# Kernel tuning notes

Measured on AMD Instinct MI355X. Metric: run time of the kernel, lower is better.

The kernel has to match this reference:

```python
import jax, jax.numpy as jnp
import numpy as np

CLASSES = 128
M_IN = 64
N_OUT = 32
N_SAMPLES = 65536


def setup_inputs() -> dict:
    key = jax.random.key(0)
    k1, k2, k3, k4 = jax.random.split(key, 4)
    x = jax.random.normal(k1, (N_SAMPLES, M_IN), dtype=jnp.float32)
    inds = jax.random.randint(k2, (N_SAMPLES,), 0, CLASSES, dtype=jnp.int64)
    # Conv2d(in=M_IN, out=CLASSES*N_OUT, kernel=1) -> weight (CLASSES*N_OUT, M_IN), bias (CLASSES*N_OUT,)
    bound = 1.0 / np.sqrt(M_IN)
    W = jax.random.uniform(k3, (CLASSES * N_OUT, M_IN), minval=-bound, maxval=bound, dtype=jnp.float32)
    b = jax.random.uniform(k4, (CLASSES * N_OUT,), minval=-bound, maxval=bound, dtype=jnp.float32)
    return {"x": x, "inds": inds, "W": W, "b": b}


def reference(x, inds, W, b):
    # 1x1 conv == GEMM: (N, m) @ (m, classes*n) + bias -> (N, classes*n)
    y = jnp.einsum("nm,cm->nc", x, W) + b  # (N, classes*n_out)
    y = y.reshape(-1, CLASSES, N_OUT)       # (N, classes, n_out)
    # gather the selected class slice per sample
    idx = inds.astype(jnp.int32)[:, None, None]  # (N, 1, 1)
    out = jnp.take_along_axis(y, jnp.broadcast_to(idx, (y.shape[0], 1, N_OUT)), axis=1)
    return out.reshape(-1, N_OUT)
```

## Files before the change

kernel.cpp:

```cpp
#include <hip/hip_runtime.h>

#define CLASSES    128
#define M_IN       64
#define N_OUT      32
#define N_SAMPLES  65536
#define BUCKET_CAP N_SAMPLES

typedef __attribute__((ext_vector_type(8))) short bf16x8;
typedef __attribute__((ext_vector_type(4))) float f32x4;

__device__ inline short f2bf(float f) {
    unsigned u = __builtin_bit_cast(unsigned, f);
    u += 0x7fffu + ((u >> 16) & 1u);
    return (short)(u >> 16);
}

__device__ inline bf16x8 cvt8(const float4 a, const float4 b) {
    bf16x8 r;
    r[0] = f2bf(a.x); r[1] = f2bf(a.y); r[2] = f2bf(a.z); r[3] = f2bf(a.w);
    r[4] = f2bf(b.x); r[5] = f2bf(b.y); r[6] = f2bf(b.z); r[7] = f2bf(b.w);
    return r;
}

__global__ __launch_bounds__(128) void zero_cnt_kernel(int* __restrict__ cnt) {
    cnt[threadIdx.x] = 0;
}

__global__ __launch_bounds__(256) void scatter_kernel(
    const int* __restrict__ inds,
    int*       __restrict__ cnt,
    int*       __restrict__ bucket)
{
    __shared__ int lcnt[CLASSES];
    __shared__ int lbase[CLASSES];
    const int tid = threadIdx.x;
    if (tid < CLASSES) lcnt[tid] = 0;
    __syncthreads();

    const int i    = blockIdx.x * 256 + tid;
    const int c    = inds[i];
    const int lpos = atomicAdd(&lcnt[c], 1);
    __syncthreads();

    if (tid < CLASSES) lbase[tid] = atomicAdd(&cnt[tid], lcnt[tid]);
    __syncthreads();

    bucket[c * BUCKET_CAP + lbase[c] + lpos] = i;
}

__global__ __launch_bounds__(256) void compute_kernel(
    const float* __restrict__ x,
    const float* __restrict__ W,
    const float* __restrict__ b,
    const int*   __restrict__ cnt,
    const int*   __restrict__ bucket,
    float*       __restrict__ out)
{
    const int c    = blockIdx.x >> 3;
    const int j8   = blockIdx.x & 7;
    const int wv   = threadIdx.x >> 6;
    const int lane = threadIdx.x & 63;
    const int m16  = lane & 15;
    const int quad = lane >> 4;

    bf16x8 Bf[2][2];
#pragma unroll
    for (int nh = 0; nh < 2; ++nh)
#pragma unroll
        for (int kh = 0; kh < 2; ++kh) {
            const float* p = W + (size_t)(c * N_OUT + nh * 16 + m16) * M_IN
                               + kh * 32 + quad * 8;
            Bf[nh][kh] = cvt8(*(const float4*)p, *(const float4*)(p + 4));
        }

    const float b0 = b[c * N_OUT + m16];
    const float b1 = b[c * N_OUT + 16 + m16];

    const int cn = cnt[c];
    if (cn == 0) return;
    const int T = (cn + 15) >> 4;
    const int* bk = bucket + c * BUCKET_CAP;

    for (int t = j8 * 4 + wv; t < T; t += 32) {
        const int base = t << 4;

        const int pa = base + m16;
        const int na = bk[(pa < cn) ? pa : (cn - 1)];
        const float* xr = x + (size_t)na * M_IN + quad * 8;
        const bf16x8 A0 = cvt8(*(const float4*)xr,        *(const float4*)(xr + 4));
        const bf16x8 A1 = cvt8(*(const float4*)(xr + 32), *(const float4*)(xr + 36));

        f32x4 acc0 = {0.f, 0.f, 0.f, 0.f};
        f32x4 acc1 = {0.f, 0.f, 0.f, 0.f};
        acc0 = __builtin_amdgcn_mfma_f32_16x16x32_bf16(A0, Bf[0][0], acc0, 0, 0, 0);
        acc0 = __builtin_amdgcn_mfma_f32_16x16x32_bf16(A1, Bf[0][1], acc0, 0, 0, 0);
        acc1 = __builtin_amdgcn_mfma_f32_16x16x32_bf16(A0, Bf[1][0], acc1, 0, 0, 0);
        acc1 = __builtin_amdgcn_mfma_f32_16x16x32_bf16(A1, Bf[1][1], acc1, 0, 0, 0);

#pragma unroll
        for (int r = 0; r < 4; ++r) {
            const int p = base + quad * 4 + r;
            if (p < cn) {
                const int n = bk[p];
                out[(size_t)n * N_OUT + m16]      = acc0[r] + b0;
                out[(size_t)n * N_OUT + 16 + m16] = acc1[r] + b1;
            }
        }
    }
}

extern "C" void kernel_launch(void* const* d_in, const int* in_sizes, int n_in,
                              void* d_out, int out_size, void* d_ws, size_t ws_size,
                              hipStream_t stream) {
    const float* x    = (const float*)d_in[0];
    const int*   inds = (const int*)  d_in[1];
    const float* W    = (const float*)d_in[2];
    const float* b    = (const float*)d_in[3];
    float*       out  = (float*)d_out;

    int* cnt    = (int*)d_ws;
    int* bucket = (int*)d_ws + 1024;

    zero_cnt_kernel<<<1, 128, 0, stream>>>(cnt);
    scatter_kernel<<<N_SAMPLES / 256, 256, 0, stream>>>(inds, cnt, bucket);
    compute_kernel<<<CLASSES * 8, 256, 0, stream>>>(x, W, b, cnt, bucket, out);
}
```

Baseline: 83.97 us.

## Prefetch next tile in compute loop, halve grids, vectorize scatter, memset counters

The compute kernel now loads the next tile's gathered x rows before it runs the MFMAs and stores for the current tile, a software-pipelining step meant to hide gather latency. The compute grid drops to 4 blocks per class, so each wave handles more tiles. The scatter kernel reads two indices per thread as an int2, and the zero-counter kernel becomes hipMemsetAsync. The int2 read treats the int64 index buffer as pairs of int32, which only works if the indices really arrive as int32. Fewer blocks may also reduce latency hiding.

```diff
diff --git a/kernel.cpp b/kernel.cpp
--- a/kernel.cpp
+++ b/kernel.cpp
@@ -22,10 +22,6 @@
     return r;
 }
 
-__global__ __launch_bounds__(128) void zero_cnt_kernel(int* __restrict__ cnt) {
-    cnt[threadIdx.x] = 0;
-}
-
 __global__ __launch_bounds__(256) void scatter_kernel(
     const int* __restrict__ inds,
     int*       __restrict__ cnt,
@@ -37,15 +33,18 @@
     if (tid < CLASSES) lcnt[tid] = 0;
     __syncthreads();
 
-    const int i    = blockIdx.x * 256 + tid;
-    const int c    = inds[i];
-    const int lpos = atomicAdd(&lcnt[c], 1);
+    const int  vi = blockIdx.x * 256 + tid;
+    const int2 cc = reinterpret_cast<const int2*>(inds)[vi];
+    const int  i0 = vi * 2, i1 = i0 + 1;
+    const int  p0 = atomicAdd(&lcnt[cc.x], 1);
+    const int  p1 = atomicAdd(&lcnt[cc.y], 1);
     __syncthreads();
 
     if (tid < CLASSES) lbase[tid] = atomicAdd(&cnt[tid], lcnt[tid]);
     __syncthreads();
 
-    bucket[c * BUCKET_CAP + lbase[c] + lpos] = i;
+    bucket[cc.x * BUCKET_CAP + lbase[cc.x] + p0] = i0;
+    bucket[cc.y * BUCKET_CAP + lbase[cc.y] + p1] = i1;
 }
 
 __global__ __launch_bounds__(256) void compute_kernel(
@@ -56,12 +55,15 @@
     const int*   __restrict__ bucket,
     float*       __restrict__ out)
 {
-    const int c    = blockIdx.x >> 3;
-    const int j8   = blockIdx.x & 7;
+    const int c    = blockIdx.x >> 2;
+    const int j4   = blockIdx.x & 3;
     const int wv   = threadIdx.x >> 6;
     const int lane = threadIdx.x & 63;
     const int m16  = lane & 15;
     const int quad = lane >> 4;
+
+    const int  cn = cnt[c];
+    const int* bk = bucket + c * BUCKET_CAP;
 
     bf16x8 Bf[2][2];
 #pragma unroll
@@ -72,24 +74,40 @@
                                + kh * 32 + quad * 8;
             Bf[nh][kh] = cvt8(*(const float4*)p, *(const float4*)(p + 4));
         }
-
     const float b0 = b[c * N_OUT + m16];
     const float b1 = b[c * N_OUT + 16 + m16];
 
-    const int cn = cnt[c];
     if (cn == 0) return;
     const int T = (cn + 15) >> 4;
-    const int* bk = bucket + c * BUCKET_CAP;
+    int t = j4 * 4 + wv;
+    if (t >= T) return;
 
-    for (int t = j8 * 4 + wv; t < T; t += 32) {
-        const int base = t << 4;
+    int base = t << 4;
+    {
+    }
+    int pa = base + m16;
+    int na = bk[(pa < cn) ? pa : (cn - 1)];
+    const float* xr = x + (size_t)na * M_IN + quad * 8;
+    float4 xa0 = *(const float4*)xr,        xa1 = *(const float4*)(xr + 4);
+    float4 xa2 = *(const float4*)(xr + 32), xa3 = *(const float4*)(xr + 36);
 
-        const int pa = base + m16;
-        const int na = bk[(pa < cn) ? pa : (cn - 1)];
-        const float* xr = x + (size_t)na * M_IN + quad * 8;
-        const bf16x8 A0 = cvt8(*(const float4*)xr,        *(const float4*)(xr + 4));
-        const bf16x8 A1 = cvt8(*(const float4*)(xr + 32), *(const float4*)(xr + 36));
+    while (true) {
+        const int  tn   = t + 16;
+        const bool more = tn < T;
 
+        int base_n = base, na_n = na;
+        float4 xb0 = xa0, xb1 = xa1, xb2 = xa2, xb3 = xa3;
+        if (more) {
+            base_n = tn << 4;
+            const int pan = base_n + m16;
+            na_n = bk[(pan < cn) ? pan : (cn - 1)];
+            const float* xrn = x + (size_t)na_n * M_IN + quad * 8;
+            xb0 = *(const float4*)xrn;        xb1 = *(const float4*)(xrn + 4);
+            xb2 = *(const float4*)(xrn + 32); xb3 = *(const float4*)(xrn + 36);
+        }
+
+        const bf16x8 A0 = cvt8(xa0, xa1);
+        const bf16x8 A1 = cvt8(xa2, xa3);
         f32x4 acc0 = {0.f, 0.f, 0.f, 0.f};
         f32x4 acc1 = {0.f, 0.f, 0.f, 0.f};
         acc0 = __builtin_amdgcn_mfma_f32_16x16x32_bf16(A0, Bf[0][0], acc0, 0, 0, 0);
@@ -106,6 +124,10 @@
                 out[(size_t)n * N_OUT + 16 + m16] = acc1[r] + b1;
             }
         }
+
+        if (!more) break;
+        t = tn; base = base_n; na = na_n;
+        xa0 = xb0; xa1 = xb1; xa2 = xb2; xa3 = xb3;
     }
 }
 
@@ -121,7 +143,7 @@
     int* cnt    = (int*)d_ws;
     int* bucket = (int*)d_ws + 1024;
 
-    zero_cnt_kernel<<<1, 128, 0, stream>>>(cnt);
-    scatter_kernel<<<N_SAMPLES / 256, 256, 0, stream>>>(inds, cnt, bucket);
-    compute_kernel<<<CLASSES * 8, 256, 0, stream>>>(x, W, b, cnt, bucket, out);
+    hipMemsetAsync(cnt, 0, CLASSES * sizeof(int), stream);
+    scatter_kernel<<<N_SAMPLES / 512, 256, 0, stream>>>(inds, cnt, bucket);
+    compute_kernel<<<CLASSES * 4, 256, 0, stream>>>(x, W, b, cnt, bucket, out);
 }
```

Result: faster. 80.91 us (-3.6%).
